# Performance work log

Measured on AMD Instinct MI355X. Metric: run time of the kernel, lower is better.

Reference implementation:

```python
import jax, jax.numpy as jnp
import numpy as np

B, A, C, D = 64, 1024, 64, 512
NEG = -9.0e15


def _ln(x, w, b, eps=1e-5):
    mu = jnp.mean(x, axis=-1, keepdims=True)
    var = jnp.mean((x - mu) ** 2, axis=-1, keepdims=True)
    return (x - mu) * jax.lax.rsqrt(var + eps) * w + b


def setup_inputs() -> dict:
    key = jax.random.key(0)
    ks = jax.random.split(key, 8)
    att_index = np.arange(A) % C
    am = np.zeros((C, A), np.float32)
    am[att_index, np.arange(A)] = 1.0 / (A // C)  # avgmask[i,j]=1/count if att_index[j]==i
    adj_ha = np.concatenate([am, np.eye(C, dtype=np.float32)], axis=1)      # [C, A+C]
    adj_ah = np.concatenate([am.T, np.eye(A, dtype=np.float32)], axis=1)    # [A, C+A]
    w = lambda k: jax.random.normal(k, (D, D), jnp.float32) * 0.05
    ones, zeros = jnp.ones((D,), jnp.float32), jnp.zeros((D,), jnp.float32)
    return {
        "att_vf": jax.random.normal(ks[0], (B, A, D), jnp.float32) * 0.05,
        "avgmask": jnp.asarray(am), "adj_ha": jnp.asarray(adj_ha), "adj_ah": jnp.asarray(adj_ah),
        "l1_W_h2h": w(ks[1]), "l1_W_h2a": w(ks[2]),
        "l1_ln1_w": ones, "l1_ln1_b": zeros, "l1_ln2_w": ones, "l1_ln2_b": zeros,
        "l1_ln3_w": ones, "l1_ln3_b": zeros,
        "l2_W_a2h": w(ks[3]), "l2_W_h2h": w(ks[4]), "l2_W_h2a": w(ks[5]),
        "l2_ln1_w": ones, "l2_ln1_b": zeros, "l2_ln2_w": ones, "l2_ln2_b": zeros,
        "l2_ln3_w": ones, "l2_ln3_b": zeros,
    }


def _forward(att_vf, avgmask, adj_ha, adj_ah,
             l1_W_h2h, l1_W_h2a, l1_ln1_w, l1_ln1_b, l1_ln2_w, l1_ln2_b, l1_ln3_w, l1_ln3_b,
             l2_W_a2h, l2_W_h2h, l2_W_h2a, l2_ln1_w, l2_ln1_b, l2_ln2_w, l2_ln2_b, l2_ln3_w, l2_ln3_b):
    inv_sd = 1.0 / jnp.sqrt(jnp.float32(D))  # input_dim == h_dim == D

    def h2h(hl, W, lw, lb):
        hln = _ln(hl, lw, lb)                                  # [B,C,D]
        hide = hln @ W
        s = jnp.einsum('bid,bjd->bij', hide, hide) * inv_sd
        a = jax.nn.softmax(s, axis=-1)
        return jnp.einsum('bij,bjd->bid', a, hln)

    def h2a(upd_hl, att, W, lw, lb):
        hln = _ln(upd_hl, lw, lb)
        hidden = jnp.concatenate([hln @ W, att], axis=1)       # [B, C+A, D]
        s = jnp.einsum('bad,bkd->bak', att, hidden) * inv_sd   # [B, A, C+A]
        s = jnp.where(adj_ah > 0, s, NEG)
        a = jax.nn.softmax(s, axis=-1)
        return jnp.einsum('bak,bkd->bad', a, hidden)

    # layer 1: a2h = 'avg'
    hl = jnp.einsum('ca,bad->bcd', avgmask, _ln(att_vf, l1_ln1_w, l1_ln1_b))  # [B,C,D]
    hl1 = h2h(hl, l1_W_h2h, l1_ln2_w, l1_ln2_b)
    att1 = h2a(hl1, att_vf, l1_W_h2a, l1_ln3_w, l1_ln3_b)

    # layer 2: a2h = 'attention'
    att_ln = _ln(att1, l2_ln1_w, l2_ln1_b)
    hidden = jnp.concatenate([att_ln @ l2_W_a2h, hl1], axis=1)  # [B, A+C, D]
    s = jnp.einsum('bcd,bkd->bck', hl1, hidden) * inv_sd        # [B, C, A+C]
    s = jnp.where(adj_ha > 0, s, NEG)
    hl2 = jnp.einsum('bck,bkd->bcd', jax.nn.softmax(s, axis=-1), hidden)
    hl2 = h2h(hl2, l2_W_h2h, l2_ln2_w, l2_ln2_b)
    att2 = h2a(hl2, att1, l2_W_h2a, l2_ln3_w, l2_ln3_b)
    return att2


def reference(att_vf, avgmask, adj_ha, adj_ah,
              l1_W_h2h, l1_W_h2a, l1_ln1_w, l1_ln1_b, l1_ln2_w, l1_ln2_b, l1_ln3_w, l1_ln3_b,
              l2_W_a2h, l2_W_h2h, l2_W_h2a, l2_ln1_w, l2_ln1_b, l2_ln2_w, l2_ln2_b, l2_ln3_w, l2_ln3_b):
    return _forward(att_vf, avgmask, adj_ha, adj_ah,
                    l1_W_h2h, l1_W_h2a, l1_ln1_w, l1_ln1_b, l1_ln2_w, l1_ln2_b, l1_ln3_w, l1_ln3_b,
                    l2_W_a2h, l2_W_h2h, l2_W_h2a, l2_ln1_w, l2_ln1_b, l2_ln2_w, l2_ln2_b, l2_ln3_w, l2_ln3_b)
```

## Files before the change

### kernel.cpp

```cpp
#include <hip/hip_runtime.h>

#define B_ 64
#define A_ 1024
#define C_ 64
#define D_ 512
#define INV_SD 0.044194173824159216f

typedef __bf16 bf16_t;
typedef __bf16 bf16x8 __attribute__((ext_vector_type(8)));
typedef __bf16 bf16x2 __attribute__((ext_vector_type(2)));
typedef float f32x4 __attribute__((ext_vector_type(4)));

static __device__ __forceinline__ bf16_t f2b(float x) { return (bf16_t)x; }
static __device__ __forceinline__ float b2f(bf16_t x) { return (float)x; }

static __device__ __forceinline__ void gl_lds16(const void* g, void* l) {
  __builtin_amdgcn_global_load_lds(
      (const __attribute__((address_space(1))) unsigned int*)g,
      (__attribute__((address_space(3))) unsigned int*)l, 16, 0, 0);
}

__global__ __launch_bounds__(256) void k_hl0(const float* __restrict__ att,
                                             const float* __restrict__ lw1,
                                             const float* __restrict__ lb1,
                                             const float* __restrict__ lw2,
                                             const float* __restrict__ lb2,
                                             bf16_t* __restrict__ hlnb) {
  int blk = blockIdx.x;
  int b = blk >> 6, c = blk & 63;
  int t = threadIdx.x;
  int w = t >> 6, lane = t & 63;
  __shared__ float part[4][512];
  __shared__ float reds[8];
  float ps[8] = {0.f, 0.f, 0.f, 0.f, 0.f, 0.f, 0.f, 0.f};
#pragma unroll
  for (int i = 0; i < 4; ++i) {
    int jj = w * 4 + i;
    const float* xr = att + ((size_t)b * A_ + jj * 64 + c) * D_ + lane * 8;
    float4 v1 = *(const float4*)xr;
    float4 v2 = *(const float4*)(xr + 4);
    float v[8] = {v1.x, v1.y, v1.z, v1.w, v2.x, v2.y, v2.z, v2.w};
    float s = 0.f, q = 0.f;
#pragma unroll
    for (int u = 0; u < 8; ++u) { s += v[u]; q += v[u] * v[u]; }
#pragma unroll
    for (int o = 32; o; o >>= 1) { s += __shfl_xor(s, o); q += __shfl_xor(q, o); }
    float mu = s * (1.0f / D_);
    float rs = rsqrtf(q * (1.0f / D_) - mu * mu + 1e-5f);
#pragma unroll
    for (int u = 0; u < 8; ++u) ps[u] += (v[u] - mu) * rs;
  }
#pragma unroll
  for (int u = 0; u < 8; ++u) part[w][lane * 8 + u] = ps[u];
  __syncthreads();
  int d = 2 * t;
  float hx = ((part[0][d] + part[1][d]) + (part[2][d] + part[3][d])) * (1.f / 16.f) * lw1[d] + lb1[d];
  float hy = ((part[0][d + 1] + part[1][d + 1]) + (part[2][d + 1] + part[3][d + 1])) * (1.f / 16.f) * lw1[d + 1] + lb1[d + 1];
  float s = hx + hy, q = hx * hx + hy * hy;
#pragma unroll
  for (int o = 32; o; o >>= 1) { s += __shfl_xor(s, o); q += __shfl_xor(q, o); }
  if (lane == 0) { reds[w] = s; reds[4 + w] = q; }
  __syncthreads();
  float S = (reds[0] + reds[1]) + (reds[2] + reds[3]);
  float Q = (reds[4] + reds[5]) + (reds[6] + reds[7]);
  float mu = S * (1.0f / D_);
  float rs = rsqrtf(Q * (1.0f / D_) - mu * mu + 1e-5f);
  bf16x2 ob;
  ob.x = f2b((hx - mu) * rs * lw2[d] + lb2[d]);
  ob.y = f2b((hy - mu) * rs * lw2[d + 1] + lb2[d + 1]);
  *(bf16x2*)(hlnb + (size_t)blk * D_ + d) = ob;
}

__global__ __launch_bounds__(256) void k_ln_tr(const bf16_t* __restrict__ x,
                                               const float* __restrict__ lw,
                                               const float* __restrict__ lb,
                                               bf16_t* __restrict__ y,
                                               bf16_t* __restrict__ yt) {
  __shared__ bf16_t lnS[64][528];
  int b = blockIdx.x;
  int t = threadIdx.x;
  int wv = t >> 6, lane = t & 63;
  int d0 = lane * 8;
  float4 w1 = *(const float4*)(lw + d0);
  float4 w2 = *(const float4*)(lw + d0 + 4);
  float4 b1 = *(const float4*)(lb + d0);
  float4 b2 = *(const float4*)(lb + d0 + 4);
  float lwv[8] = {w1.x, w1.y, w1.z, w1.w, w2.x, w2.y, w2.z, w2.w};
  float lbv[8] = {b1.x, b1.y, b1.z, b1.w, b2.x, b2.y, b2.z, b2.w};
  const bf16_t* xb = x + (size_t)b * C_ * D_;
  bf16_t* yb = y + (size_t)b * C_ * D_;
#pragma unroll 4
  for (int i = 0; i < 16; ++i) {
    int r = wv * 16 + i;
    bf16x8 xv = *(const bf16x8*)(xb + (size_t)r * D_ + d0);
    float v[8], s = 0.f, q = 0.f;
#pragma unroll
    for (int u = 0; u < 8; ++u) { v[u] = b2f(xv[u]); s += v[u]; q += v[u] * v[u]; }
#pragma unroll
    for (int o = 32; o; o >>= 1) { s += __shfl_xor(s, o); q += __shfl_xor(q, o); }
    float mu = s * (1.0f / D_);
    float rs = rsqrtf(q * (1.0f / D_) - mu * mu + 1e-5f);
    bf16x8 ob;
#pragma unroll
    for (int u = 0; u < 8; ++u) ob[u] = f2b((v[u] - mu) * rs * lwv[u] + lbv[u]);
    *(bf16x8*)(yb + (size_t)r * D_ + d0) = ob;
    *(bf16x8*)(&lnS[r][d0]) = ob;
  }
  __syncthreads();
  bf16_t* tb = yt + (size_t)b * D_ * C_;
#pragma unroll
  for (int pass = 0; pass < 16; ++pass) {
    int d = pass * 32 + (t >> 3);
    int c0 = (t & 7) * 8;
    unsigned short tmp[8];
#pragma unroll
    for (int u = 0; u < 8; ++u) tmp[u] = *(const unsigned short*)&lnS[c0 + u][d];
    *(uint4*)(tb + (size_t)d * 64 + c0) = *(const uint4*)tmp;
  }
}

__global__ __launch_bounds__(256) void k_tr(const bf16_t* __restrict__ src,
                                            bf16_t* __restrict__ dst) {
  __shared__ unsigned short sm[64][72];
  int n0 = blockIdx.x;
  int b = blockIdx.y;
  int t = threadIdx.x;
  const bf16_t* sb = src + (size_t)b * C_ * D_;
  bf16_t* db = dst + (size_t)b * D_ * C_;
#pragma unroll
  for (int rep = 0; rep < 2; ++rep) {
    int f = t + rep * 256;
    int r = f >> 3, c8 = f & 7;
    uint4 v = *(const uint4*)(sb + (size_t)r * D_ + n0 * 64 + c8 * 8);
    unsigned int* p = (unsigned int*)&sm[r][c8 * 8];
    p[0] = v.x; p[1] = v.y; p[2] = v.z; p[3] = v.w;
  }
  __syncthreads();
#pragma unroll
  for (int rep = 0; rep < 2; ++rep) {
    int f = t + rep * 256;
    int nr = f >> 3, c8 = f & 7;
    unsigned short tmp[8];
#pragma unroll
    for (int u = 0; u < 8; ++u) tmp[u] = sm[c8 * 8 + u][nr];
    *(uint4*)(db + (size_t)(n0 * 64 + nr) * 64 + c8 * 8) = *(const uint4*)tmp;
  }
}

__global__ __launch_bounds__(256) void k_wt6(const float* __restrict__ W0, const float* __restrict__ W1,
                                             const float* __restrict__ W2, const float* __restrict__ W3,
                                             const float* __restrict__ W4, bf16_t* __restrict__ WtBase) {
  __shared__ float tile[64][65];
  const float* Ws[5] = {W0, W1, W2, W3, W4};
  int z = blockIdx.z;
  int k0 = blockIdx.x * 64;
  int n0 = blockIdx.y * 64;
  int t = threadIdx.x;
  int r0 = t >> 6;
  int c = t & 63;
  if (z == 5) {
    const float* W = Ws[2];
    bf16_t* Wt = WtBase + (size_t)5 * 512 * 512;
#pragma unroll 4
    for (int i = 0; i < 16; ++i) {
      int r = r0 * 16 + i;
      Wt[(size_t)(k0 + r) * 512 + n0 + c] = f2b(W[(size_t)(k0 + r) * 512 + n0 + c]);
    }
    return;
  }
  const float* W = Ws[z];
  bf16_t* Wt = WtBase + (size_t)z * 512 * 512;
#pragma unroll 4
  for (int i = 0; i < 16; ++i) {
    int r = r0 * 16 + i;
    tile[r][c] = W[(size_t)(k0 + r) * 512 + n0 + c];
  }
  __syncthreads();
#pragma unroll 4
  for (int i = 0; i < 16; ++i) {
    int r = r0 * 16 + i;
    Wt[(size_t)(n0 + r) * 512 + k0 + c] = f2b(tile[c][r]);
  }
}

template <bool BIAS>
__global__ __launch_bounds__(256, 4) void k_gemm64(const bf16_t* __restrict__ A0,
                                                   const bf16_t* __restrict__ W0,
                                                   bf16_t* __restrict__ C0,
                                                   const bf16_t* __restrict__ A1,
                                                   const bf16_t* __restrict__ W1,
                                                   bf16_t* __restrict__ C1,
                                                   const bf16_t* __restrict__ Rb,
                                                   int tiles_per) {
  constexpr int ABYTES = 64 * 128;
  constexpr int BUF = 2 * ABYTES;
  __shared__ char smem[2 * BUF];

  int t = threadIdx.x;
  int lane = t & 63, wave = t >> 6;
  int wr = wave >> 1, wc = wave & 1;
  int lhi = lane >> 4, llo = lane & 15;

  int nwg = gridDim.x;
  int bid = blockIdx.x;
  int tile = (bid & 7) * (nwg >> 3) + (bid >> 3);
  int sel = (tile >= tiles_per) ? 1 : 0;
  int tidx = tile - sel * tiles_per;
  int bm = tidx >> 3, bn = tidx & 7;

  const bf16_t* Ab = (sel ? A1 : A0) + (size_t)bm * 64 * 512;
  const bf16_t* Wb = (sel ? W1 : W0) + (size_t)bn * 64 * 512;
  bf16_t* Cmat = sel ? C1 : C0;

  int l3 = lane >> 3;
  int srcOff = ((lane & 7) ^ l3) * 8;

  auto stage = [&](int k0, int bi) {
    char* As = smem + bi * BUF;
    char* Bs = As + ABYTES;
#pragma unroll
    for (int i = 0; i < 2; ++i) {
      int r0 = wave * 16 + i * 8;
      gl_lds16(Ab + (size_t)(r0 + l3) * 512 + k0 + srcOff, As + r0 * 128);
      gl_lds16(Wb + (size_t)(r0 + l3) * 512 + k0 + srcOff, Bs + r0 * 128);
    }
  };

  f32x4 acc[2][2] = {};
  stage(0, 0);
  __syncthreads();

  for (int it = 0; it < 8; ++it) {
    int cur = it & 1;
    if (it < 7) stage((it + 1) * 64, cur ^ 1);
    const char* As = smem + cur * BUF;
    const char* Bs = As + ABYTES;
#pragma unroll
    for (int kk = 0; kk < 2; ++kk) {
      bf16x8 af[2], bfr[2];
      int bofs = kk * 64 + lhi * 16;
#pragma unroll
      for (int tr = 0; tr < 2; ++tr) {
        int row = wr * 32 + tr * 16 + llo;
        af[tr] = *(const bf16x8*)(As + row * 128 + (bofs ^ ((row & 7) << 4)));
      }
#pragma unroll
      for (int tc = 0; tc < 2; ++tc) {
        int col = wc * 32 + tc * 16 + llo;
        bfr[tc] = *(const bf16x8*)(Bs + col * 128 + (bofs ^ ((col & 7) << 4)));
      }
#pragma unroll
      for (int tr = 0; tr < 2; ++tr)
#pragma unroll
        for (int tc = 0; tc < 2; ++tc)
          acc[tr][tc] = __builtin_amdgcn_mfma_f32_16x16x32_bf16(af[tr], bfr[tc], acc[tr][tc], 0, 0, 0);
    }
    __syncthreads();
  }

  bf16_t(*Cs)[80] = (bf16_t(*)[80])smem;
#pragma unroll
  for (int tr = 0; tr < 2; ++tr) {
    int row = wr * 32 + tr * 16 + lhi * 4;
#pragma unroll
    for (int r = 0; r < 4; ++r)
#pragma unroll
      for (int tc = 0; tc < 2; ++tc) {
        float v = acc[tr][tc][r];
        if constexpr (BIAS)
          v += b2f(Rb[(size_t)(bm * 64 + row + r) * 512 + bn * 64 + wc * 32 + tc * 16 + llo]);
        Cs[row + r][wc * 32 + tc * 16 + llo] = f2b(v);
      }
  }
  __syncthreads();
#pragma unroll
  for (int it = 0; it < 2; ++it) {
    int idx = t + it * 256;
    int row = idx >> 3, c8 = idx & 7;
    uint4 v = *(const uint4*)(&Cs[row][c8 * 8]);
    *(uint4*)(Cmat + (size_t)(bm * 64 + row) * 512 + bn * 64 + c8 * 8) = v;
  }
}

template <int MODE>
__global__ __launch_bounds__(256) void k_h2h(const bf16_t* __restrict__ hide,
                                             const bf16_t* __restrict__ hlnT,
                                             const float* __restrict__ lnw,
                                             const float* __restrict__ lnbv,
                                             float* __restrict__ hl1f,
                                             bf16_t* __restrict__ hl1b,
                                             bf16_t* __restrict__ lnout) {
  __shared__ bf16_t hS[8 * 64 * 64];
  __shared__ float sS[16][68];
  __shared__ bf16_t wS[16 * 64];
  __shared__ float mur[16], rsr[16];

  int q = blockIdx.x;
  int b = blockIdx.y;
  int t = threadIdx.x;
  int lane = t & 63, wave = t >> 6;
  int lhi = lane >> 4, llo = lane & 15;

  const bf16_t* Hb = hide + (size_t)b * C_ * D_;
#pragma unroll
  for (int rep = 0; rep < 16; ++rep) {
    int f = t + rep * 256;
    int row = f >> 6, c16 = f & 63;
    int kc = c16 >> 3, ci = c16 & 7;
    uint4 v = *(const uint4*)(Hb + (size_t)row * 512 + c16 * 8);
    *(uint4*)((char*)hS + kc * 8192 + row * 128 + ((ci * 16) ^ ((row & 7) << 4))) = v;
  }
  __syncthreads();

  {
    f32x4 acc = {};
#pragma unroll
    for (int ks = 0; ks < 16; ++ks) {
      int kc = ks >> 1;
      int bofs = (ks & 1) * 64 + lhi * 16;
      int ra = q * 16 + llo;
      int rb = wave * 16 + llo;
      bf16x8 af = *(const bf16x8*)((const char*)hS + kc * 8192 + ra * 128 + (bofs ^ ((ra & 7) << 4)));
      bf16x8 bf = *(const bf16x8*)((const char*)hS + kc * 8192 + rb * 128 + (bofs ^ ((rb & 7) << 4)));
      acc = __builtin_amdgcn_mfma_f32_16x16x32_bf16(af, bf, acc, 0, 0, 0);
    }
#pragma unroll
    for (int r = 0; r < 4; ++r) sS[lhi * 4 + r][wave * 16 + llo] = acc[r] * INV_SD;
  }
  __syncthreads();

  if (t < 128) {
    int row = t >> 3, sg = t & 7;
    float v[8];
#pragma unroll
    for (int u = 0; u < 8; ++u) v[u] = sS[row][sg * 8 + u];
    float m = v[0];
#pragma unroll
    for (int u = 1; u < 8; ++u) m = fmaxf(m, v[u]);
#pragma unroll
    for (int o = 4; o; o >>= 1) m = fmaxf(m, __shfl_xor(m, o));
    float sum = 0.f;
#pragma unroll
    for (int u = 0; u < 8; ++u) { v[u] = __expf(v[u] - m); sum += v[u]; }
#pragma unroll
    for (int o = 4; o; o >>= 1) sum += __shfl_xor(sum, o);
    float inv = 1.f / sum;
    bf16x8 wv;
#pragma unroll
    for (int u = 0; u < 8; ++u) wv[u] = f2b(v[u] * inv);
    *(bf16x8*)((char*)wS + row * 128 + ((sg * 16) ^ ((row & 7) << 4))) = wv;
  }
  __syncthreads();

  float* sf = (float*)hS;
  {
    bf16x8 af[2];
#pragma unroll
    for (int ks = 0; ks < 2; ++ks)
      af[ks] = *(const bf16x8*)((const char*)wS + llo * 128 + (((ks * 64 + lhi * 16)) ^ ((llo & 7) << 4)));
    const bf16_t* Tb = hlnT + (size_t)b * D_ * C_;
#pragma unroll
    for (int nt = 0; nt < 8; ++nt) {
      int dcol = wave * 128 + nt * 16 + llo;
      f32x4 acc = {};
#pragma unroll
      for (int ks = 0; ks < 2; ++ks) {
        bf16x8 bf = *(const bf16x8*)(Tb + (size_t)dcol * 64 + ks * 32 + lhi * 8);
        acc = __builtin_amdgcn_mfma_f32_16x16x32_bf16(af[ks], bf, acc, 0, 0, 0);
      }
#pragma unroll
      for (int r = 0; r < 4; ++r) sf[(lhi * 4 + r) * 516 + dcol] = acc[r];
    }
  }
  __syncthreads();

  {
    int lr = t >> 4, p = t & 15;
    float s = 0.f, q2 = 0.f;
#pragma unroll 8
    for (int i = 0; i < 32; ++i) {
      float v = sf[lr * 516 + p + 16 * i];
      s += v;
      q2 += v * v;
    }
#pragma unroll
    for (int o = 8; o; o >>= 1) { s += __shfl_xor(s, o); q2 += __shfl_xor(q2, o); }
    if (p == 0) {
      float mu = s * (1.0f / D_);
      mur[lr] = mu;
      rsr[lr] = rsqrtf(q2 * (1.0f / D_) - mu * mu + 1e-5f);
    }
  }
  __syncthreads();

  int d = 2 * t;
  float lwx = lnw[d], lwy = lnw[d + 1], lbx = lnbv[d], lby = lnbv[d + 1];
#pragma unroll 4
  for (int r = 0; r < 16; ++r) {
    float2 xy = *(const float2*)(&sf[r * 516 + d]);
    size_t go = ((size_t)b * C_ + q * 16 + r) * 512 + d;
    float mu = mur[r], rs = rsr[r];
    if constexpr (MODE == 0) {
      *(float2*)(hl1f + go) = xy;
      bf16x2 hb;
      hb.x = f2b(xy.x);
      hb.y = f2b(xy.y);
      *(bf16x2*)(hl1b + go) = hb;
    }
    bf16x2 lb2;
    lb2.x = f2b((xy.x - mu) * rs * lwx + lbx);
    lb2.y = f2b((xy.y - mu) * rs * lwy + lby);
    *(bf16x2*)(lnout + go) = lb2;
  }
}

__global__ __launch_bounds__(256) void k_h2a_ln(const float* __restrict__ att,
                                                const bf16_t* __restrict__ hW,
                                                bf16_t* __restrict__ att1b,
                                                float* __restrict__ stats) {
  int t = threadIdx.x;
  int row = blockIdx.x * 4 + (t >> 6);
  int lane = t & 63;
  int b = row >> 10, a = row & 1023;
  int c = a & 63;
  int d0 = lane * 8;
  const float* ar = att + (size_t)row * D_ + d0;
  const bf16_t* wr = hW + (size_t)(b * 64 + c) * D_ + d0;
  float4 a1 = *(const float4*)ar;
  float4 a2 = *(const float4*)(ar + 4);
  bf16x8 wb = *(const bf16x8*)wr;
  float w[8], av[8] = {a1.x, a1.y, a1.z, a1.w, a2.x, a2.y, a2.z, a2.w};
#pragma unroll
  for (int u = 0; u < 8; ++u) w[u] = b2f(wb[u]);
  float d1 = 0.f, d2 = 0.f;
#pragma unroll
  for (int u = 0; u < 8; ++u) { d1 += av[u] * w[u]; d2 += av[u] * av[u]; }
#pragma unroll
  for (int o = 32; o; o >>= 1) { d1 += __shfl_xor(d1, o); d2 += __shfl_xor(d2, o); }
  float s1 = d1 * INV_SD, s2 = d2 * INV_SD;
  float m = fmaxf(s1, s2);
  float e1 = __expf(s1 - m), e2 = __expf(s2 - m);
  float inv = 1.f / (e1 + e2);
  float alpha = e1 * inv, beta = e2 * inv;
  float o8[8];
  float s = 0.f, q = 0.f;
#pragma unroll
  for (int u = 0; u < 8; ++u) {
    o8[u] = alpha * w[u] + beta * av[u];
    s += o8[u];
    q += o8[u] * o8[u];
  }
  bf16x8 ob;
#pragma unroll
  for (int u = 0; u < 8; ++u) ob[u] = f2b(o8[u]);
  *(bf16x8*)(att1b + (size_t)row * D_ + d0) = ob;
#pragma unroll
  for (int o = 32; o; o >>= 1) { s += __shfl_xor(s, o); q += __shfl_xor(q, o); }
  if (lane == 0) {
    float mu = s * (1.0f / D_);
    stats[2 * row] = mu;
    stats[2 * row + 1] = rsqrtf(q * (1.0f / D_) - mu * mu + 1e-5f);
  }
}

__global__ __launch_bounds__(256) void k_h2a_out(const bf16_t* __restrict__ att,
                                                 const bf16_t* __restrict__ hW,
                                                 float* __restrict__ outp) {
  int t = threadIdx.x;
  int row = blockIdx.x * 4 + (t >> 6);
  int lane = t & 63;
  int b = row >> 10, a = row & 1023;
  int c = a & 63;
  int d0 = lane * 8;
  bf16x8 ab = *(const bf16x8*)(att + (size_t)row * D_ + d0);
  bf16x8 wb = *(const bf16x8*)(hW + (size_t)(b * 64 + c) * D_ + d0);
  float av[8], w[8];
#pragma unroll
  for (int u = 0; u < 8; ++u) { av[u] = b2f(ab[u]); w[u] = b2f(wb[u]); }
  float d1 = 0.f, d2 = 0.f;
#pragma unroll
  for (int u = 0; u < 8; ++u) { d1 += av[u] * w[u]; d2 += av[u] * av[u]; }
#pragma unroll
  for (int o = 32; o; o >>= 1) { d1 += __shfl_xor(d1, o); d2 += __shfl_xor(d2, o); }
  float s1 = d1 * INV_SD, s2 = d2 * INV_SD;
  float m = fmaxf(s1, s2);
  float e1 = __expf(s1 - m), e2 = __expf(s2 - m);
  float inv = 1.f / (e1 + e2);
  float alpha = e1 * inv, beta = e2 * inv;
  float4 o1, o2;
  o1.x = alpha * w[0] + beta * av[0]; o1.y = alpha * w[1] + beta * av[1];
  o1.z = alpha * w[2] + beta * av[2]; o1.w = alpha * w[3] + beta * av[3];
  o2.x = alpha * w[4] + beta * av[4]; o2.y = alpha * w[5] + beta * av[5];
  o2.z = alpha * w[6] + beta * av[6]; o2.w = alpha * w[7] + beta * av[7];
  float* orow = outp + (size_t)row * D_ + d0;
  *(float4*)orow = o1;
  *(float4*)(orow + 4) = o2;
}

__global__ __launch_bounds__(256) void k_a2h_u(const float* __restrict__ hl1f,
                                               const bf16_t* __restrict__ G,
                                               const bf16_t* __restrict__ att1b,
                                               const float* __restrict__ stats,
                                               const float* __restrict__ lw,
                                               const float* __restrict__ lb,
                                               bf16_t* __restrict__ u_out,
                                               bf16_t* __restrict__ R_out) {
  int blk = blockIdx.x;
  int b = blk >> 6, c = blk & 63;
  int t = threadIdx.x;
  int wave = t >> 6, lane = t & 63;
  __shared__ float hrow[512], grow[512], lwS[512], lbS[512];
  __shared__ bf16_t lnS[16][512];
  __shared__ float wts[32];
  __shared__ float red[4];
  {
    int d = 2 * t;
    float2 h2 = *(const float2*)(hl1f + (size_t)blk * 512 + d);
    hrow[d] = h2.x;
    hrow[d + 1] = h2.y;
    bf16x2 g2 = *(const bf16x2*)(G + (size_t)blk * 512 + d);
    grow[d] = b2f(g2.x);
    grow[d + 1] = b2f(g2.y);
    float2 w2 = *(const float2*)(lw + d);
    lwS[d] = w2.x;
    lwS[d + 1] = w2.y;
    float2 bb = *(const float2*)(lb + d);
    lbS[d] = bb.x;
    lbS[d + 1] = bb.y;
    float sd = h2.x * h2.x + h2.y * h2.y;
#pragma unroll
    for (int o = 32; o; o >>= 1) sd += __shfl_xor(sd, o);
    if (lane == 0) red[wave] = sd;
  }
  __syncthreads();
#pragma unroll
  for (int i = 0; i < 4; ++i) {
    int j = wave * 4 + i;
    size_t row = (size_t)b * A_ + j * 64 + c;
    float mu = stats[2 * row], rs = stats[2 * row + 1];
    bf16x8 x = *(const bf16x8*)(att1b + row * 512 + lane * 8);
    float dot = 0.f;
    bf16x8 lnv;
#pragma unroll
    for (int u = 0; u < 8; ++u) {
      int k = lane * 8 + u;
      float v = (b2f(x[u]) - mu) * rs * lwS[k] + lbS[k];
      lnv[u] = f2b(v);
      dot += v * grow[k];
    }
    *(bf16x8*)(&lnS[j][lane * 8]) = lnv;
#pragma unroll
    for (int o = 32; o; o >>= 1) dot += __shfl_xor(dot, o);
    if (lane == 0) wts[j] = dot * INV_SD;
  }
  if (t == 0) wts[16] = ((red[0] + red[1]) + (red[2] + red[3])) * INV_SD;
  __syncthreads();
  if (t < 64) {
    float val = (t < 17) ? wts[t] : -3.0e38f;
    float m = val;
#pragma unroll
    for (int o = 32; o; o >>= 1) m = fmaxf(m, __shfl_xor(m, o));
    float e = (t < 17) ? __expf(val - m) : 0.f;
    float ssum = e;
#pragma unroll
    for (int o = 32; o; o >>= 1) ssum += __shfl_xor(ssum, o);
    if (t < 17) wts[t] = e / ssum;
  }
  __syncthreads();
  int d = 2 * t;
  float ux = 0.f, uy = 0.f;
#pragma unroll 4
  for (int jj = 0; jj < 16; ++jj) {
    bf16x2 l2 = *(const bf16x2*)(&lnS[jj][d]);
    ux += wts[jj] * b2f(l2.x);
    uy += wts[jj] * b2f(l2.y);
  }
  bf16x2 uo, ro;
  uo.x = f2b(ux);
  uo.y = f2b(uy);
  *(bf16x2*)(u_out + (size_t)blk * 512 + d) = uo;
  float w16 = wts[16];
  ro.x = f2b(w16 * hrow[d]);
  ro.y = f2b(w16 * hrow[d + 1]);
  *(bf16x2*)(R_out + (size_t)blk * 512 + d) = ro;
}

extern "C" void kernel_launch(void* const* d_in, const int* in_sizes, int n_in,
                              void* d_out, int out_size, void* d_ws, size_t ws_size,
                              hipStream_t stream) {
  const float* att_vf = (const float*)d_in[0];
  const float* W1_h2h = (const float*)d_in[4];
  const float* W1_h2a = (const float*)d_in[5];
  const float* ln11w = (const float*)d_in[6];
  const float* ln11b = (const float*)d_in[7];
  const float* ln12w = (const float*)d_in[8];
  const float* ln12b = (const float*)d_in[9];
  const float* ln13w = (const float*)d_in[10];
  const float* ln13b = (const float*)d_in[11];
  const float* W2_a2h = (const float*)d_in[12];
  const float* W2_h2h = (const float*)d_in[13];
  const float* W2_h2a = (const float*)d_in[14];
  const float* ln21w = (const float*)d_in[15];
  const float* ln21b = (const float*)d_in[16];
  const float* ln22w = (const float*)d_in[17];
  const float* ln22b = (const float*)d_in[18];
  const float* ln23w = (const float*)d_in[19];
  const float* ln23b = (const float*)d_in[20];
  float* out = (float*)d_out;

  float* ws = (float*)d_ws;
  const size_t SM = (size_t)B_ * C_ * D_;
  float* hl1f = ws;
  bf16_t* A1b = (bf16_t*)(hl1f + SM);
  bf16_t* A1t = (bf16_t*)((float*)A1b + SM / 2);
  bf16_t* A2b = (bf16_t*)((float*)A1t + SM / 2);
  bf16_t* hl1b = (bf16_t*)((float*)A2b + SM / 2);
  bf16_t* u_b = (bf16_t*)((float*)hl1b + SM / 2);
  bf16_t* R_b = (bf16_t*)((float*)u_b + SM / 2);
  bf16_t* Gb = (bf16_t*)((float*)R_b + SM / 2);
  bf16_t* Wt0 = (bf16_t*)((float*)Gb + SM / 2);
  const size_t WTE = (size_t)512 * 512;
  bf16_t* att1b = Wt0 + 6 * WTE;
  float* stats = (float*)(att1b + (size_t)B_ * A_ * D_);

  dim3 blk(256);
  k_wt6<<<dim3(8, 8, 6), blk, 0, stream>>>(W1_h2h, W1_h2a, W2_a2h, W2_h2h, W2_h2a, Wt0);

  k_hl0<<<B_ * C_, blk, 0, stream>>>(att_vf, ln11w, ln11b, ln12w, ln12b, A1b);
  k_tr<<<dim3(8, B_), blk, 0, stream>>>(A1b, A1t);
  k_gemm64<false><<<512, blk, 0, stream>>>(A1b, Wt0 + 0 * WTE, A2b,
                                           A1b, Wt0 + 0 * WTE, A2b, nullptr, 512);
  k_h2h<0><<<dim3(4, B_), blk, 0, stream>>>(A2b, A1t, ln13w, ln13b, hl1f, hl1b, A1b);
  k_gemm64<false><<<1024, blk, 0, stream>>>(A1b, Wt0 + 1 * WTE, A2b,
                                            hl1b, Wt0 + 5 * WTE, Gb, nullptr, 512);
  k_h2a_ln<<<(B_ * A_) / 4, blk, 0, stream>>>(att_vf, A2b, att1b, stats);
  k_a2h_u<<<B_ * C_, blk, 0, stream>>>(hl1f, Gb, att1b, stats, ln21w, ln21b, u_b, R_b);
  k_gemm64<true><<<512, blk, 0, stream>>>(u_b, Wt0 + 2 * WTE, A2b,
                                          u_b, Wt0 + 2 * WTE, A2b, R_b, 512);
  k_ln_tr<<<B_, blk, 0, stream>>>(A2b, ln22w, ln22b, A1b, A1t);
  k_gemm64<false><<<512, blk, 0, stream>>>(A1b, Wt0 + 3 * WTE, A2b,
                                           A1b, Wt0 + 3 * WTE, A2b, nullptr, 512);
  k_h2h<1><<<dim3(4, B_), blk, 0, stream>>>(A2b, A1t, ln23w, ln23b, nullptr, nullptr, A1b);
  k_gemm64<false><<<512, blk, 0, stream>>>(A1b, Wt0 + 4 * WTE, A2b,
                                           A1b, Wt0 + 4 * WTE, A2b, nullptr, 512);
  k_h2a_out<<<(B_ * A_) / 4, blk, 0, stream>>>(att1b, A2b, out);
}
```

Before: 196.9 us.

## Merge prep kernels, fold transpose into GEMM grid, fuse h2a_ln with a2h

Combines weight transpose/convert with the initial layer-norm pooling into one launch. The standalone transpose kernel now runs as extra blocks appended to the first GEMM grid. The h2a softmax/LN kernel and the a2h pooling kernel are merged so att1 is normalized in registers, which removes the stats buffer and the re-read of att1b. This cuts launch count and one full pass over the B*A*D bf16 tensor, but the fused kernel has fewer blocks per row of work and mixed block types may unbalance occupancy.

```diff
diff --git a/kernel.cpp b/kernel.cpp
--- a/kernel.cpp
+++ b/kernel.cpp
@@ -20,55 +20,96 @@
       (__attribute__((address_space(3))) unsigned int*)l, 16, 0, 0);
 }
 
-__global__ __launch_bounds__(256) void k_hl0(const float* __restrict__ att,
-                                             const float* __restrict__ lw1,
-                                             const float* __restrict__ lb1,
-                                             const float* __restrict__ lw2,
-                                             const float* __restrict__ lb2,
-                                             bf16_t* __restrict__ hlnb) {
-  int blk = blockIdx.x;
-  int b = blk >> 6, c = blk & 63;
+__global__ __launch_bounds__(256) void k_prep(const float* __restrict__ att,
+                                              const float* __restrict__ lw1,
+                                              const float* __restrict__ lb1,
+                                              const float* __restrict__ lw2,
+                                              const float* __restrict__ lb2,
+                                              bf16_t* __restrict__ hlnb,
+                                              const float* __restrict__ W0,
+                                              const float* __restrict__ W1,
+                                              const float* __restrict__ W2,
+                                              const float* __restrict__ W3,
+                                              const float* __restrict__ W4,
+                                              bf16_t* __restrict__ WtBase) {
+  __shared__ float shm[64 * 65];
+  __shared__ float reds[8];
+  int bid = blockIdx.x;
   int t = threadIdx.x;
-  int w = t >> 6, lane = t & 63;
-  __shared__ float part[4][512];
-  __shared__ float reds[8];
-  float ps[8] = {0.f, 0.f, 0.f, 0.f, 0.f, 0.f, 0.f, 0.f};
-#pragma unroll
-  for (int i = 0; i < 4; ++i) {
-    int jj = w * 4 + i;
-    const float* xr = att + ((size_t)b * A_ + jj * 64 + c) * D_ + lane * 8;
-    float4 v1 = *(const float4*)xr;
-    float4 v2 = *(const float4*)(xr + 4);
-    float v[8] = {v1.x, v1.y, v1.z, v1.w, v2.x, v2.y, v2.z, v2.w};
-    float s = 0.f, q = 0.f;
-#pragma unroll
-    for (int u = 0; u < 8; ++u) { s += v[u]; q += v[u] * v[u]; }
+  if (bid < B_ * C_) {
+    int b = bid >> 6, c = bid & 63;
+    int w = t >> 6, lane = t & 63;
+    float (*part)[512] = (float(*)[512])shm;
+    float ps[8] = {0.f, 0.f, 0.f, 0.f, 0.f, 0.f, 0.f, 0.f};
+#pragma unroll
+    for (int i = 0; i < 4; ++i) {
+      int jj = w * 4 + i;
+      const float* xr = att + ((size_t)b * A_ + jj * 64 + c) * D_ + lane * 8;
+      float4 v1 = *(const float4*)xr;
+      float4 v2 = *(const float4*)(xr + 4);
+      float v[8] = {v1.x, v1.y, v1.z, v1.w, v2.x, v2.y, v2.z, v2.w};
+      float s = 0.f, q = 0.f;
+#pragma unroll
+      for (int u = 0; u < 8; ++u) { s += v[u]; q += v[u] * v[u]; }
+#pragma unroll
+      for (int o = 32; o; o >>= 1) { s += __shfl_xor(s, o); q += __shfl_xor(q, o); }
+      float mu = s * (1.0f / D_);
+      float rs = rsqrtf(q * (1.0f / D_) - mu * mu + 1e-5f);
+#pragma unroll
+      for (int u = 0; u < 8; ++u) ps[u] += (v[u] - mu) * rs;
+    }
+#pragma unroll
+    for (int u = 0; u < 8; ++u) part[w][lane * 8 + u] = ps[u];
+    __syncthreads();
+    int d = 2 * t;
+    float hx = ((part[0][d] + part[1][d]) + (part[2][d] + part[3][d])) * (1.f / 16.f) * lw1[d] + lb1[d];
+    float hy = ((part[0][d + 1] + part[1][d + 1]) + (part[2][d + 1] + part[3][d + 1])) * (1.f / 16.f) * lw1[d + 1] + lb1[d + 1];
+    float s = hx + hy, q = hx * hx + hy * hy;
 #pragma unroll
     for (int o = 32; o; o >>= 1) { s += __shfl_xor(s, o); q += __shfl_xor(q, o); }
-    float mu = s * (1.0f / D_);
-    float rs = rsqrtf(q * (1.0f / D_) - mu * mu + 1e-5f);
-#pragma unroll
-    for (int u = 0; u < 8; ++u) ps[u] += (v[u] - mu) * rs;
-  }
-#pragma unroll
-  for (int u = 0; u < 8; ++u) part[w][lane * 8 + u] = ps[u];
-  __syncthreads();
-  int d = 2 * t;
-  float hx = ((part[0][d] + part[1][d]) + (part[2][d] + part[3][d])) * (1.f / 16.f) * lw1[d] + lb1[d];
-  float hy = ((part[0][d + 1] + part[1][d + 1]) + (part[2][d + 1] + part[3][d + 1])) * (1.f / 16.f) * lw1[d + 1] + lb1[d + 1];
-  float s = hx + hy, q = hx * hx + hy * hy;
-#pragma unroll
-  for (int o = 32; o; o >>= 1) { s += __shfl_xor(s, o); q += __shfl_xor(q, o); }
-  if (lane == 0) { reds[w] = s; reds[4 + w] = q; }
-  __syncthreads();
-  float S = (reds[0] + reds[1]) + (reds[2] + reds[3]);
-  float Q = (reds[4] + reds[5]) + (reds[6] + reds[7]);
-  float mu = S * (1.0f / D_);
-  float rs = rsqrtf(Q * (1.0f / D_) - mu * mu + 1e-5f);
-  bf16x2 ob;
-  ob.x = f2b((hx - mu) * rs * lw2[d] + lb2[d]);
-  ob.y = f2b((hy - mu) * rs * lw2[d + 1] + lb2[d + 1]);
-  *(bf16x2*)(hlnb + (size_t)blk * D_ + d) = ob;
+    if (lane == 0) { reds[w] = s; reds[4 + w] = q; }
+    __syncthreads();
+    float S = (reds[0] + reds[1]) + (reds[2] + reds[3]);
+    float Q = (reds[4] + reds[5]) + (reds[6] + reds[7]);
+    float mu = S * (1.0f / D_);
+    float rs = rsqrtf(Q * (1.0f / D_) - mu * mu + 1e-5f);
+    bf16x2 ob;
+    ob.x = f2b((hx - mu) * rs * lw2[d] + lb2[d]);
+    ob.y = f2b((hy - mu) * rs * lw2[d + 1] + lb2[d + 1]);
+    *(bf16x2*)(hlnb + (size_t)bid * D_ + d) = ob;
+  } else {
+    int idx = bid - B_ * C_;
+    int z = idx >> 6;
+    int rem = idx & 63;
+    int k0 = (rem & 7) * 64, n0 = (rem >> 3) * 64;
+    const float* Ws[5] = {W0, W1, W2, W3, W4};
+    int r0 = t >> 6;
+    int c = t & 63;
+    if (z == 5) {
+      const float* W = Ws[2];
+      bf16_t* Wt = WtBase + (size_t)5 * 512 * 512;
+#pragma unroll 4
+      for (int i = 0; i < 16; ++i) {
+        int r = r0 * 16 + i;
+        Wt[(size_t)(k0 + r) * 512 + n0 + c] = f2b(W[(size_t)(k0 + r) * 512 + n0 + c]);
+      }
+      return;
+    }
+    const float* W = Ws[z];
+    bf16_t* Wt = WtBase + (size_t)z * 512 * 512;
+    float (*tile)[65] = (float(*)[65])shm;
+#pragma unroll 4
+    for (int i = 0; i < 16; ++i) {
+      int r = r0 * 16 + i;
+      tile[r][c] = W[(size_t)(k0 + r) * 512 + n0 + c];
+    }
+    __syncthreads();
+#pragma unroll 4
+    for (int i = 0; i < 16; ++i) {
+      int r = r0 * 16 + i;
+      Wt[(size_t)(n0 + r) * 512 + k0 + c] = f2b(tile[c][r]);
+    }
+  }
 }
 
 __global__ __launch_bounds__(256) void k_ln_tr(const bf16_t* __restrict__ x,
@@ -119,70 +160,6 @@
   }
 }
 
-__global__ __launch_bounds__(256) void k_tr(const bf16_t* __restrict__ src,
-                                            bf16_t* __restrict__ dst) {
-  __shared__ unsigned short sm[64][72];
-  int n0 = blockIdx.x;
-  int b = blockIdx.y;
-  int t = threadIdx.x;
-  const bf16_t* sb = src + (size_t)b * C_ * D_;
-  bf16_t* db = dst + (size_t)b * D_ * C_;
-#pragma unroll
-  for (int rep = 0; rep < 2; ++rep) {
-    int f = t + rep * 256;
-    int r = f >> 3, c8 = f & 7;
-    uint4 v = *(const uint4*)(sb + (size_t)r * D_ + n0 * 64 + c8 * 8);
-    unsigned int* p = (unsigned int*)&sm[r][c8 * 8];
-    p[0] = v.x; p[1] = v.y; p[2] = v.z; p[3] = v.w;
-  }
-  __syncthreads();
-#pragma unroll
-  for (int rep = 0; rep < 2; ++rep) {
-    int f = t + rep * 256;
-    int nr = f >> 3, c8 = f & 7;
-    unsigned short tmp[8];
-#pragma unroll
-    for (int u = 0; u < 8; ++u) tmp[u] = sm[c8 * 8 + u][nr];
-    *(uint4*)(db + (size_t)(n0 * 64 + nr) * 64 + c8 * 8) = *(const uint4*)tmp;
-  }
-}
-
-__global__ __launch_bounds__(256) void k_wt6(const float* __restrict__ W0, const float* __restrict__ W1,
-                                             const float* __restrict__ W2, const float* __restrict__ W3,
-                                             const float* __restrict__ W4, bf16_t* __restrict__ WtBase) {
-  __shared__ float tile[64][65];
-  const float* Ws[5] = {W0, W1, W2, W3, W4};
-  int z = blockIdx.z;
-  int k0 = blockIdx.x * 64;
-  int n0 = blockIdx.y * 64;
-  int t = threadIdx.x;
-  int r0 = t >> 6;
-  int c = t & 63;
-  if (z == 5) {
-    const float* W = Ws[2];
-    bf16_t* Wt = WtBase + (size_t)5 * 512 * 512;
-#pragma unroll 4
-    for (int i = 0; i < 16; ++i) {
-      int r = r0 * 16 + i;
-      Wt[(size_t)(k0 + r) * 512 + n0 + c] = f2b(W[(size_t)(k0 + r) * 512 + n0 + c]);
-    }
-    return;
-  }
-  const float* W = Ws[z];
-  bf16_t* Wt = WtBase + (size_t)z * 512 * 512;
-#pragma unroll 4
-  for (int i = 0; i < 16; ++i) {
-    int r = r0 * 16 + i;
-    tile[r][c] = W[(size_t)(k0 + r) * 512 + n0 + c];
-  }
-  __syncthreads();
-#pragma unroll 4
-  for (int i = 0; i < 16; ++i) {
-    int r = r0 * 16 + i;
-    Wt[(size_t)(n0 + r) * 512 + k0 + c] = f2b(tile[c][r]);
-  }
-}
-
 template <bool BIAS>
 __global__ __launch_bounds__(256, 4) void k_gemm64(const bf16_t* __restrict__ A0,
                                                    const bf16_t* __restrict__ W0,
@@ -191,19 +168,48 @@
                                                    const bf16_t* __restrict__ W1,
                                                    bf16_t* __restrict__ C1,
                                                    const bf16_t* __restrict__ Rb,
-                                                   int tiles_per) {
+                                                   int tiles_per, int ntiles,
+                                                   const bf16_t* __restrict__ trS,
+                                                   bf16_t* __restrict__ trD) {
   constexpr int ABYTES = 64 * 128;
   constexpr int BUF = 2 * ABYTES;
   __shared__ char smem[2 * BUF];
 
   int t = threadIdx.x;
+  int bid = blockIdx.x;
+
+  if (bid >= ntiles) {
+    int idx = bid - ntiles;
+    int n0 = idx & 7, b = idx >> 3;
+    unsigned short(*sm)[72] = (unsigned short(*)[72])smem;
+    const bf16_t* sb = trS + (size_t)b * C_ * D_;
+    bf16_t* db = trD + (size_t)b * D_ * C_;
+#pragma unroll
+    for (int rep = 0; rep < 2; ++rep) {
+      int f = t + rep * 256;
+      int r = f >> 3, c8 = f & 7;
+      uint4 v = *(const uint4*)(sb + (size_t)r * D_ + n0 * 64 + c8 * 8);
+      unsigned int* p = (unsigned int*)&sm[r][c8 * 8];
+      p[0] = v.x; p[1] = v.y; p[2] = v.z; p[3] = v.w;
+    }
+    __syncthreads();
+#pragma unroll
+    for (int rep = 0; rep < 2; ++rep) {
+      int f = t + rep * 256;
+      int nr = f >> 3, c8 = f & 7;
+      unsigned short tmp[8];
+#pragma unroll
+      for (int u = 0; u < 8; ++u) tmp[u] = sm[c8 * 8 + u][nr];
+      *(uint4*)(db + (size_t)(n0 * 64 + nr) * 64 + c8 * 8) = *(const uint4*)tmp;
+    }
+    return;
+  }
+
   int lane = t & 63, wave = t >> 6;
   int wr = wave >> 1, wc = wave & 1;
   int lhi = lane >> 4, llo = lane & 15;
 
-  int nwg = gridDim.x;
-  int bid = blockIdx.x;
-  int tile = (bid & 7) * (nwg >> 3) + (bid >> 3);
+  int tile = (bid & 7) * (ntiles >> 3) + (bid >> 3);
   int sel = (tile >= tiles_per) ? 1 : 0;
   int tidx = tile - sel * tiles_per;
   int bm = tidx >> 3, bn = tidx & 7;
@@ -414,53 +420,123 @@
   }
 }
 
-__global__ __launch_bounds__(256) void k_h2a_ln(const float* __restrict__ att,
+__global__ __launch_bounds__(256) void k_l2head(const float* __restrict__ att,
                                                 const bf16_t* __restrict__ hW,
+                                                const float* __restrict__ hl1f,
+                                                const bf16_t* __restrict__ G,
+                                                const float* __restrict__ lw,
+                                                const float* __restrict__ lb,
                                                 bf16_t* __restrict__ att1b,
-                                                float* __restrict__ stats) {
+                                                bf16_t* __restrict__ u_out,
+                                                bf16_t* __restrict__ R_out) {
+  int blk = blockIdx.x;
+  int b = blk >> 6, c = blk & 63;
   int t = threadIdx.x;
-  int row = blockIdx.x * 4 + (t >> 6);
-  int lane = t & 63;
-  int b = row >> 10, a = row & 1023;
-  int c = a & 63;
+  int w = t >> 6, lane = t & 63;
   int d0 = lane * 8;
-  const float* ar = att + (size_t)row * D_ + d0;
-  const bf16_t* wr = hW + (size_t)(b * 64 + c) * D_ + d0;
-  float4 a1 = *(const float4*)ar;
-  float4 a2 = *(const float4*)(ar + 4);
-  bf16x8 wb = *(const bf16x8*)wr;
-  float w[8], av[8] = {a1.x, a1.y, a1.z, a1.w, a2.x, a2.y, a2.z, a2.w};
-#pragma unroll
-  for (int u = 0; u < 8; ++u) w[u] = b2f(wb[u]);
-  float d1 = 0.f, d2 = 0.f;
-#pragma unroll
-  for (int u = 0; u < 8; ++u) { d1 += av[u] * w[u]; d2 += av[u] * av[u]; }
-#pragma unroll
-  for (int o = 32; o; o >>= 1) { d1 += __shfl_xor(d1, o); d2 += __shfl_xor(d2, o); }
-  float s1 = d1 * INV_SD, s2 = d2 * INV_SD;
-  float m = fmaxf(s1, s2);
-  float e1 = __expf(s1 - m), e2 = __expf(s2 - m);
-  float inv = 1.f / (e1 + e2);
-  float alpha = e1 * inv, beta = e2 * inv;
-  float o8[8];
-  float s = 0.f, q = 0.f;
-#pragma unroll
-  for (int u = 0; u < 8; ++u) {
-    o8[u] = alpha * w[u] + beta * av[u];
-    s += o8[u];
-    q += o8[u] * o8[u];
-  }
-  bf16x8 ob;
-#pragma unroll
-  for (int u = 0; u < 8; ++u) ob[u] = f2b(o8[u]);
-  *(bf16x8*)(att1b + (size_t)row * D_ + d0) = ob;
-#pragma unroll
-  for (int o = 32; o; o >>= 1) { s += __shfl_xor(s, o); q += __shfl_xor(q, o); }
-  if (lane == 0) {
+  __shared__ bf16_t lnS[16][512];
+  __shared__ float hrow[512];
+  __shared__ float wts[32];
+  __shared__ float red[4];
+
+  {
+    int d = 2 * t;
+    float2 h2 = *(const float2*)(hl1f + (size_t)blk * 512 + d);
+    hrow[d] = h2.x;
+    hrow[d + 1] = h2.y;
+    float sd = h2.x * h2.x + h2.y * h2.y;
+#pragma unroll
+    for (int o = 32; o; o >>= 1) sd += __shfl_xor(sd, o);
+    if (lane == 0) red[w] = sd;
+  }
+  bf16x8 wb = *(const bf16x8*)(hW + (size_t)blk * 512 + d0);
+  bf16x8 gb = *(const bf16x8*)(G + (size_t)blk * 512 + d0);
+  float wv[8], gv[8];
+#pragma unroll
+  for (int u = 0; u < 8; ++u) { wv[u] = b2f(wb[u]); gv[u] = b2f(gb[u]); }
+  float4 w1 = *(const float4*)(lw + d0);
+  float4 w2 = *(const float4*)(lw + d0 + 4);
+  float4 b1 = *(const float4*)(lb + d0);
+  float4 b2 = *(const float4*)(lb + d0 + 4);
+  float lwv[8] = {w1.x, w1.y, w1.z, w1.w, w2.x, w2.y, w2.z, w2.w};
+  float lbv[8] = {b1.x, b1.y, b1.z, b1.w, b2.x, b2.y, b2.z, b2.w};
+
+#pragma unroll
+  for (int i = 0; i < 4; ++i) {
+    int j = w * 4 + i;
+    size_t row = (size_t)b * A_ + j * 64 + c;
+    const float* ar = att + row * 512 + d0;
+    float4 a1 = *(const float4*)ar;
+    float4 a2 = *(const float4*)(ar + 4);
+    float av[8] = {a1.x, a1.y, a1.z, a1.w, a2.x, a2.y, a2.z, a2.w};
+    float d1 = 0.f, d2 = 0.f;
+#pragma unroll
+    for (int u = 0; u < 8; ++u) { d1 += av[u] * wv[u]; d2 += av[u] * av[u]; }
+#pragma unroll
+    for (int o = 32; o; o >>= 1) { d1 += __shfl_xor(d1, o); d2 += __shfl_xor(d2, o); }
+    float s1 = d1 * INV_SD, s2 = d2 * INV_SD;
+    float m = fmaxf(s1, s2);
+    float e1 = __expf(s1 - m), e2 = __expf(s2 - m);
+    float inv = 1.f / (e1 + e2);
+    float alpha = e1 * inv, beta = e2 * inv;
+    float o8[8], s = 0.f, q = 0.f;
+    bf16x8 ob;
+#pragma unroll
+    for (int u = 0; u < 8; ++u) {
+      o8[u] = alpha * wv[u] + beta * av[u];
+      s += o8[u];
+      q += o8[u] * o8[u];
+      ob[u] = f2b(o8[u]);
+    }
+    *(bf16x8*)(att1b + row * 512 + d0) = ob;
+#pragma unroll
+    for (int o = 32; o; o >>= 1) { s += __shfl_xor(s, o); q += __shfl_xor(q, o); }
     float mu = s * (1.0f / D_);
-    stats[2 * row] = mu;
-    stats[2 * row + 1] = rsqrtf(q * (1.0f / D_) - mu * mu + 1e-5f);
-  }
+    float rs = rsqrtf(q * (1.0f / D_) - mu * mu + 1e-5f);
+    float dot = 0.f;
+    bf16x8 lnv;
+#pragma unroll
+    for (int u = 0; u < 8; ++u) {
+      float v = (o8[u] - mu) * rs * lwv[u] + lbv[u];
+      lnv[u] = f2b(v);
+      dot += v * gv[u];
+    }
+    *(bf16x8*)(&lnS[j][d0]) = lnv;
+#pragma unroll
+    for (int o = 32; o; o >>= 1) dot += __shfl_xor(dot, o);
+    if (lane == 0) wts[j] = dot * INV_SD;
+  }
+  __syncthreads();
+  if (t == 0) wts[16] = ((red[0] + red[1]) + (red[2] + red[3])) * INV_SD;
+  __syncthreads();
+  if (t < 64) {
+    float val = (t < 17) ? wts[t] : -3.0e38f;
+    float m = val;
+#pragma unroll
+    for (int o = 32; o; o >>= 1) m = fmaxf(m, __shfl_xor(m, o));
+    float e = (t < 17) ? __expf(val - m) : 0.f;
+    float ssum = e;
+#pragma unroll
+    for (int o = 32; o; o >>= 1) ssum += __shfl_xor(ssum, o);
+    if (t < 17) wts[t] = e / ssum;
+  }
+  __syncthreads();
+  int d = 2 * t;
+  float ux = 0.f, uy = 0.f;
+#pragma unroll 4
+  for (int jj = 0; jj < 16; ++jj) {
+    bf16x2 l2 = *(const bf16x2*)(&lnS[jj][d]);
+    ux += wts[jj] * b2f(l2.x);
+    uy += wts[jj] * b2f(l2.y);
+  }
+  bf16x2 uo, ro;
+  uo.x = f2b(ux);
+  uo.y = f2b(uy);
+  *(bf16x2*)(u_out + (size_t)blk * 512 + d) = uo;
+  float w16 = wts[16];
+  ro.x = f2b(w16 * hrow[d]);
+  ro.y = f2b(w16 * hrow[d + 1]);
+  *(bf16x2*)(R_out + (size_t)blk * 512 + d) = ro;
 }
 
 __global__ __launch_bounds__(256) void k_h2a_out(const bf16_t* __restrict__ att,
@@ -495,94 +571,6 @@
   float* orow = outp + (size_t)row * D_ + d0;
   *(float4*)orow = o1;
   *(float4*)(orow + 4) = o2;
-}
-
-__global__ __launch_bounds__(256) void k_a2h_u(const float* __restrict__ hl1f,
-                                               const bf16_t* __restrict__ G,
-                                               const bf16_t* __restrict__ att1b,
-                                               const float* __restrict__ stats,
-                                               const float* __restrict__ lw,
-                                               const float* __restrict__ lb,
-                                               bf16_t* __restrict__ u_out,
-                                               bf16_t* __restrict__ R_out) {
-  int blk = blockIdx.x;
-  int b = blk >> 6, c = blk & 63;
-  int t = threadIdx.x;
-  int wave = t >> 6, lane = t & 63;
-  __shared__ float hrow[512], grow[512], lwS[512], lbS[512];
-  __shared__ bf16_t lnS[16][512];
-  __shared__ float wts[32];
-  __shared__ float red[4];
-  {
-    int d = 2 * t;
-    float2 h2 = *(const float2*)(hl1f + (size_t)blk * 512 + d);
-    hrow[d] = h2.x;
-    hrow[d + 1] = h2.y;
-    bf16x2 g2 = *(const bf16x2*)(G + (size_t)blk * 512 + d);
-    grow[d] = b2f(g2.x);
-    grow[d + 1] = b2f(g2.y);
-    float2 w2 = *(const float2*)(lw + d);
-    lwS[d] = w2.x;
-    lwS[d + 1] = w2.y;
-    float2 bb = *(const float2*)(lb + d);
-    lbS[d] = bb.x;
-    lbS[d + 1] = bb.y;
-    float sd = h2.x * h2.x + h2.y * h2.y;
-#pragma unroll
-    for (int o = 32; o; o >>= 1) sd += __shfl_xor(sd, o);
-    if (lane == 0) red[wave] = sd;
-  }
-  __syncthreads();
-#pragma unroll
-  for (int i = 0; i < 4; ++i) {
-    int j = wave * 4 + i;
-    size_t row = (size_t)b * A_ + j * 64 + c;
-    float mu = stats[2 * row], rs = stats[2 * row + 1];
-    bf16x8 x = *(const bf16x8*)(att1b + row * 512 + lane * 8);
-    float dot = 0.f;
-    bf16x8 lnv;
-#pragma unroll
-    for (int u = 0; u < 8; ++u) {
-      int k = lane * 8 + u;
-      float v = (b2f(x[u]) - mu) * rs * lwS[k] + lbS[k];
-      lnv[u] = f2b(v);
-      dot += v * grow[k];
-    }
-    *(bf16x8*)(&lnS[j][lane * 8]) = lnv;
-#pragma unroll
-    for (int o = 32; o; o >>= 1) dot += __shfl_xor(dot, o);
-    if (lane == 0) wts[j] = dot * INV_SD;
-  }
-  if (t == 0) wts[16] = ((red[0] + red[1]) + (red[2] + red[3])) * INV_SD;
-  __syncthreads();
-  if (t < 64) {
-    float val = (t < 17) ? wts[t] : -3.0e38f;
-    float m = val;
-#pragma unroll
-    for (int o = 32; o; o >>= 1) m = fmaxf(m, __shfl_xor(m, o));
-    float e = (t < 17) ? __expf(val - m) : 0.f;
-    float ssum = e;
-#pragma unroll
-    for (int o = 32; o; o >>= 1) ssum += __shfl_xor(ssum, o);
-    if (t < 17) wts[t] = e / ssum;
-  }
-  __syncthreads();
-  int d = 2 * t;
-  float ux = 0.f, uy = 0.f;
-#pragma unroll 4
-  for (int jj = 0; jj < 16; ++jj) {
-    bf16x2 l2 = *(const bf16x2*)(&lnS[jj][d]);
-    ux += wts[jj] * b2f(l2.x);
-    uy += wts[jj] * b2f(l2.y);
-  }
-  bf16x2 uo, ro;
-  uo.x = f2b(ux);
-  uo.y = f2b(uy);
-  *(bf16x2*)(u_out + (size_t)blk * 512 + d) = uo;
-  float w16 = wts[16];
-  ro.x = f2b(w16 * hrow[d]);
-  ro.y = f2b(w16 * hrow[d + 1]);
-  *(bf16x2*)(R_out + (size_t)blk * 512 + d) = ro;
 }
 
 extern "C" void kernel_launch(void* const* d_in, const int* in_sizes, int n_in,
@@ -621,27 +609,28 @@
   bf16_t* Wt0 = (bf16_t*)((float*)Gb + SM / 2);
   const size_t WTE = (size_t)512 * 512;
   bf16_t* att1b = Wt0 + 6 * WTE;
-  float* stats = (float*)(att1b + (size_t)B_ * A_ * D_);
 
   dim3 blk(256);
-  k_wt6<<<dim3(8, 8, 6), blk, 0, stream>>>(W1_h2h, W1_h2a, W2_a2h, W2_h2h, W2_h2a, Wt0);
-
-  k_hl0<<<B_ * C_, blk, 0, stream>>>(att_vf, ln11w, ln11b, ln12w, ln12b, A1b);
-  k_tr<<<dim3(8, B_), blk, 0, stream>>>(A1b, A1t);
-  k_gemm64<false><<<512, blk, 0, stream>>>(A1b, Wt0 + 0 * WTE, A2b,
-                                           A1b, Wt0 + 0 * WTE, A2b, nullptr, 512);
+  k_prep<<<B_ * C_ + 384, blk, 0, stream>>>(att_vf, ln11w, ln11b, ln12w, ln12b, A1b,
+                                            W1_h2h, W1_h2a, W2_a2h, W2_h2h, W2_h2a, Wt0);
+  k_gemm64<false><<<1024, blk, 0, stream>>>(A1b, Wt0 + 0 * WTE, A2b,
+                                            A1b, Wt0 + 0 * WTE, A2b, nullptr, 512, 512,
+                                            A1b, A1t);
   k_h2h<0><<<dim3(4, B_), blk, 0, stream>>>(A2b, A1t, ln13w, ln13b, hl1f, hl1b, A1b);
   k_gemm64<false><<<1024, blk, 0, stream>>>(A1b, Wt0 + 1 * WTE, A2b,
-                                            hl1b, Wt0 + 5 * WTE, Gb, nullptr, 512);
-  k_h2a_ln<<<(B_ * A_) / 4, blk, 0, stream>>>(att_vf, A2b, att1b, stats);
-  k_a2h_u<<<B_ * C_, blk, 0, stream>>>(hl1f, Gb, att1b, stats, ln21w, ln21b, u_b, R_b);
+                                            hl1b, Wt0 + 5 * WTE, Gb, nullptr, 512, 1024,
+                                            nullptr, nullptr);
+  k_l2head<<<B_ * C_, blk, 0, stream>>>(att_vf, A2b, hl1f, Gb, ln21w, ln21b, att1b, u_b, R_b);
   k_gemm64<true><<<512, blk, 0, stream>>>(u_b, Wt0 + 2 * WTE, A2b,
-                                          u_b, Wt0 + 2 * WTE, A2b, R_b, 512);
+                                          u_b, Wt0 + 2 * WTE, A2b, R_b, 512, 512,
+                                          nullptr, nullptr);
   k_ln_tr<<<B_, blk, 0, stream>>>(A2b, ln22w, ln22b, A1b, A1t);
   k_gemm64<false><<<512, blk, 0, stream>>>(A1b, Wt0 + 3 * WTE, A2b,
-                                           A1b, Wt0 + 3 * WTE, A2b, nullptr, 512);
+                                           A1b, Wt0 + 3 * WTE, A2b, nullptr, 512, 512,
+                                           nullptr, nullptr);
   k_h2h<1><<<dim3(4, B_), blk, 0, stream>>>(A2b, A1t, ln23w, ln23b, nullptr, nullptr, A1b);
   k_gemm64<false><<<512, blk, 0, stream>>>(A1b, Wt0 + 4 * WTE, A2b,
-                                           A1b, Wt0 + 4 * WTE, A2b, nullptr, 512);
+                                           A1b, Wt0 + 4 * WTE, A2b, nullptr, 512, 512,
+                                           nullptr, nullptr);
   k_h2a_out<<<(B_ * A_) / 4, blk, 0, stream>>>(att1b, A2b, out);
 }
```

Result: faster. 180.5 us (-8.3%).
